# Kernel optimization log

Hardware: AMD Instinct MI355X
Metric: run time of the kernel (lower is better)

Reference implementation:

```python
import jax, jax.numpy as jnp
import numpy as np

N_NODES = 50000


def setup_inputs() -> dict:
    key = jax.random.key(0)
    k1, k2, k3, k4, k5, k6 = jax.random.split(key, 6)
    N, E, D, F = 50000, 800000, 512, 256
    feature_ori = jax.random.normal(k1, (N, D), dtype=jnp.float32)
    feature_aug = jax.random.normal(k2, (N, D), dtype=jnp.float32)
    edge_row = jax.random.randint(k3, (E,), 0, N, dtype=jnp.int32)
    edge_col = jax.random.randint(k4, (E,), 0, N, dtype=jnp.int32)
    edge_val = jax.random.uniform(k5, (E,), dtype=jnp.float32)
    # kaiming-uniform-ish init for weight, zeros for bias (as in reset_parameters)
    bound = float(np.sqrt(6.0 / D))
    weight = jax.random.uniform(k6, (D, F), dtype=jnp.float32, minval=-bound, maxval=bound)
    bias = jnp.zeros((F,), dtype=jnp.float32)
    return {
        "feature_ori": feature_ori,
        "feature_aug": feature_aug,
        "edge_row": edge_row,
        "edge_col": edge_col,
        "edge_val": edge_val,
        "weight": weight,
        "bias": bias,
    }


def _branch(feat, weight, bias, edge_row, edge_col, edge_val):
    # support = X @ W  -> [N, F]
    support = feat @ weight
    # sparse aggregation: out[i] = sum_{e: row[e]=i} val[e] * support[col[e]]
    msgs = edge_val[:, None] * support[edge_col]          # [E, F]
    out = jax.ops.segment_sum(msgs, edge_row, num_segments=N_NODES)
    return jax.nn.relu(out + bias)


def reference(feature_ori, feature_aug, edge_row, edge_col, edge_val, weight, bias):
    out_ori = _branch(feature_ori, weight, bias, edge_row, edge_col, edge_val)
    out_aug = _branch(feature_aug, weight, bias, edge_row, edge_col, edge_val)
    return (out_ori, out_aug)
```

## Files before the change

kernel.cpp:

```cpp
#include <hip/hip_runtime.h>
#include <hip/hip_bf16.h>

#define NNODES 50000
#define NEDGES 800000
#define DIN    512
#define FOUT   256

typedef __attribute__((ext_vector_type(8))) short short8;
typedef __attribute__((ext_vector_type(4))) float f32x4;
typedef __attribute__((ext_vector_type(4))) unsigned int u32x4;
typedef __attribute__((ext_vector_type(4))) unsigned short usv4;

static __device__ __forceinline__ unsigned short f2bf(float f) {
    unsigned int u = __float_as_uint(f);
    u += 0x7FFF + ((u >> 16) & 1);
    return (unsigned short)(u >> 16);
}
static __device__ __forceinline__ float bf2f(unsigned short h) {
    return __uint_as_float(((unsigned int)h) << 16);
}

__global__ void wt_convert(const float* __restrict__ W, unsigned short* __restrict__ Wt) {
    int o = blockIdx.x * 256 + threadIdx.x;
    int n = o >> 9, k = o & 511;
    Wt[o] = f2bf(W[k * FOUT + n]);
}

__global__ void hist_kernel(const int* __restrict__ row, int* __restrict__ cnt) {
    int e = blockIdx.x * 256 + threadIdx.x;
    if (e < NEDGES) atomicAdd(&cnt[row[e]], 1);
}

__global__ void scan_partial(const int* __restrict__ cnt, int* __restrict__ partial) {
    __shared__ int sm[256];
    int i = blockIdx.x * 256 + threadIdx.x;
    int v = (i < NNODES) ? cnt[i] : 0;
    sm[threadIdx.x] = v; __syncthreads();
    for (int s = 128; s > 0; s >>= 1) {
        if (threadIdx.x < s) sm[threadIdx.x] += sm[threadIdx.x + s];
        __syncthreads();
    }
    if (threadIdx.x == 0) partial[blockIdx.x] = sm[0];
}

__global__ void scan_exclusive_small(int* __restrict__ partial, int nb) {
    __shared__ int sm[256];
    int t = threadIdx.x;
    int v = (t < nb) ? partial[t] : 0;
    sm[t] = v; __syncthreads();
    for (int off = 1; off < 256; off <<= 1) {
        int add = (t >= off) ? sm[t - off] : 0;
        __syncthreads();
        sm[t] += add;
        __syncthreads();
    }
    if (t < nb) partial[t] = sm[t] - v;
}

__global__ void scan_write(const int* __restrict__ cnt, const int* __restrict__ partial,
                           int* __restrict__ row_start, int* __restrict__ cursor) {
    __shared__ int sm[256];
    int t = threadIdx.x;
    int i = blockIdx.x * 256 + t;
    int v = (i < NNODES) ? cnt[i] : 0;
    sm[t] = v; __syncthreads();
    for (int off = 1; off < 256; off <<= 1) {
        int add = (t >= off) ? sm[t - off] : 0;
        __syncthreads();
        sm[t] += add;
        __syncthreads();
    }
    if (i < NNODES) {
        int rs = partial[blockIdx.x] + sm[t] - v;
        row_start[i] = rs;
        cursor[i] = rs;
    }
    if (i == 0) row_start[NNODES] = NEDGES;
}

__global__ void scatter_kernel(const int* __restrict__ row, const int* __restrict__ col,
                               const float* __restrict__ val,
                               int* __restrict__ cursor, unsigned int* __restrict__ cv) {
    int e = blockIdx.x * 256 + threadIdx.x;
    if (e < NEDGES) {
        int r = row[e];
        int pos = atomicAdd(&cursor[r], 1);
        unsigned int vb = f2bf(val[e]);
        cv[pos] = (vb << 16) | (unsigned int)col[e];
    }
}

__global__ __launch_bounds__(512, 2)
void gemm_kernel(const float* __restrict__ Xo, const float* __restrict__ Xa,
                 const unsigned short* __restrict__ Wt,
                 unsigned short* __restrict__ S) {
    __shared__ __align__(16) unsigned short As[2][128][40];
    __shared__ __align__(16) unsigned short Bs[2][256][40];
    const int tid = threadIdx.x;
    const int branch = blockIdx.z;
    const float* __restrict__ X = branch ? Xa : Xo;
    const int boff = branch * 256;
    const int m_base = blockIdx.x * 128;
    const int lane = tid & 63, wave = tid >> 6;
    const int wm = (wave >> 2) * 64, wn = (wave & 3) * 64;
    const int quad = lane >> 4, r16 = lane & 15;

    f32x4 acc[4][4] = {};

    const int colf  = (tid & 7) * 4;
    const int rbase = tid >> 3;
    const int kseg  = (tid & 3) * 8;
    const int nrow  = tid >> 2;

    const int gm0 = m_base + rbase;
    const int gm1 = m_base + 64 + rbase;
    const bool va0 = gm0 < NNODES, va1 = gm1 < NNODES;
    const float* pA0 = &X[(long)gm0 * DIN + colf];
    const float* pA1 = &X[(long)gm1 * DIN + colf];
    const unsigned short* pB0 = &Wt[(long)nrow * DIN + kseg];
    const unsigned short* pB1 = &Wt[(long)(128 + nrow) * DIN + kseg];

    f32x4 fa0, fa1; u32x4 ub0, ub1;

#define GEMM_LOAD(K0)                                                          \
    do {                                                                       \
        fa0 = va0 ? __builtin_nontemporal_load((const f32x4*)(pA0 + (K0)))     \
                  : (f32x4)0.f;                                                \
        fa1 = va1 ? __builtin_nontemporal_load((const f32x4*)(pA1 + (K0)))     \
                  : (f32x4)0.f;                                                \
        ub0 = *(const u32x4*)(pB0 + (K0));                                     \
        ub1 = *(const u32x4*)(pB1 + (K0));                                     \
    } while (0)

#define GEMM_WRITE(B)                                                          \
    do {                                                                       \
        usv4 h0; h0.x = f2bf(fa0[0]); h0.y = f2bf(fa0[1]);                     \
        h0.z = f2bf(fa0[2]); h0.w = f2bf(fa0[3]);                              \
        *(usv4*)&As[B][rbase][colf] = h0;                                      \
        usv4 h1; h1.x = f2bf(fa1[0]); h1.y = f2bf(fa1[1]);                     \
        h1.z = f2bf(fa1[2]); h1.w = f2bf(fa1[3]);                              \
        *(usv4*)&As[B][64 + rbase][colf] = h1;                                 \
        *(u32x4*)&Bs[B][nrow][kseg] = ub0;                                     \
        *(u32x4*)&Bs[B][128 + nrow][kseg] = ub1;                               \
    } while (0)

#define GEMM_COMPUTE(B)                                                        \
    do {                                                                       \
        short8 a_frag[4], b_frag[4];                                           \
        _Pragma("unroll")                                                      \
        for (int mi = 0; mi < 4; mi++)                                         \
            a_frag[mi] = *(const short8*)&As[B][wm + mi * 16 + r16][quad * 8]; \
        _Pragma("unroll")                                                      \
        for (int ni = 0; ni < 4; ni++)                                         \
            b_frag[ni] = *(const short8*)&Bs[B][wn + ni * 16 + r16][quad * 8]; \
        _Pragma("unroll")                                                      \
        for (int mi = 0; mi < 4; mi++)                                         \
            _Pragma("unroll")                                                  \
            for (int ni = 0; ni < 4; ni++)                                     \
                acc[mi][ni] = __builtin_amdgcn_mfma_f32_16x16x32_bf16(         \
                    a_frag[mi], b_frag[ni], acc[mi][ni], 0, 0, 0);             \
    } while (0)

    GEMM_LOAD(0);
    GEMM_WRITE(0);
    __syncthreads();

    for (int k0 = 0; k0 < DIN; k0 += 64) {
        GEMM_LOAD(k0 + 32);
        GEMM_COMPUTE(0);
        GEMM_WRITE(1);
        __syncthreads();
        if (k0 + 64 < DIN) GEMM_LOAD(k0 + 64);
        GEMM_COMPUTE(1);
        if (k0 + 64 < DIN) GEMM_WRITE(0);
        __syncthreads();
    }

#undef GEMM_LOAD
#undef GEMM_WRITE
#undef GEMM_COMPUTE

    #pragma unroll
    for (int mi = 0; mi < 4; mi++) {
        #pragma unroll
        for (int rr = 0; rr < 4; rr++) {
            int m = m_base + wm + mi * 16 + quad * 4 + rr;
            if (m < NNODES) {
                #pragma unroll
                for (int ni = 0; ni < 4; ni++) {
                    int n = wn + ni * 16 + r16;
                    S[(long)m * 512 + boff + n] = f2bf(acc[mi][ni][rr]);
                }
            }
        }
    }
}

__global__ __launch_bounds__(256)
void aggregate_kernel(const int* __restrict__ row_start,
                      const unsigned int* __restrict__ cv,
                      const unsigned short* __restrict__ S,
                      const float* __restrict__ bias, float* __restrict__ out) {
    int node = blockIdx.x * 4 + (threadIdx.x >> 6);
    int lane = threadIdx.x & 63;
    if (node >= NNODES) return;
    int s = row_start[node], e = row_start[node + 1];
    float ao0 = 0.f, ao1 = 0.f, ao2 = 0.f, ao3 = 0.f;
    float aa0 = 0.f, aa1 = 0.f, aa2 = 0.f, aa3 = 0.f;
    const int lo = lane * 4;

    int idx = s;
    for (; idx + 4 <= e; idx += 4) {
        unsigned int w0 = __builtin_nontemporal_load(&cv[idx]);
        unsigned int w1 = __builtin_nontemporal_load(&cv[idx + 1]);
        unsigned int w2 = __builtin_nontemporal_load(&cv[idx + 2]);
        unsigned int w3 = __builtin_nontemporal_load(&cv[idx + 3]);
        const unsigned short* p0 = &S[(long)(w0 & 0xFFFFu) * 512 + lo];
        const unsigned short* p1 = &S[(long)(w1 & 0xFFFFu) * 512 + lo];
        const unsigned short* p2 = &S[(long)(w2 & 0xFFFFu) * 512 + lo];
        const unsigned short* p3 = &S[(long)(w3 & 0xFFFFu) * 512 + lo];
        usv4 po0 = *(const usv4*)p0;       usv4 pa0 = *(const usv4*)(p0 + 256);
        usv4 po1 = *(const usv4*)p1;       usv4 pa1 = *(const usv4*)(p1 + 256);
        usv4 po2 = *(const usv4*)p2;       usv4 pa2 = *(const usv4*)(p2 + 256);
        usv4 po3 = *(const usv4*)p3;       usv4 pa3 = *(const usv4*)(p3 + 256);
        float v0 = bf2f((unsigned short)(w0 >> 16));
        float v1 = bf2f((unsigned short)(w1 >> 16));
        float v2 = bf2f((unsigned short)(w2 >> 16));
        float v3 = bf2f((unsigned short)(w3 >> 16));
        ao0 += v0 * bf2f(po0.x); ao1 += v0 * bf2f(po0.y); ao2 += v0 * bf2f(po0.z); ao3 += v0 * bf2f(po0.w);
        aa0 += v0 * bf2f(pa0.x); aa1 += v0 * bf2f(pa0.y); aa2 += v0 * bf2f(pa0.z); aa3 += v0 * bf2f(pa0.w);
        ao0 += v1 * bf2f(po1.x); ao1 += v1 * bf2f(po1.y); ao2 += v1 * bf2f(po1.z); ao3 += v1 * bf2f(po1.w);
        aa0 += v1 * bf2f(pa1.x); aa1 += v1 * bf2f(pa1.y); aa2 += v1 * bf2f(pa1.z); aa3 += v1 * bf2f(pa1.w);
        ao0 += v2 * bf2f(po2.x); ao1 += v2 * bf2f(po2.y); ao2 += v2 * bf2f(po2.z); ao3 += v2 * bf2f(po2.w);
        aa0 += v2 * bf2f(pa2.x); aa1 += v2 * bf2f(pa2.y); aa2 += v2 * bf2f(pa2.z); aa3 += v2 * bf2f(pa2.w);
        ao0 += v3 * bf2f(po3.x); ao1 += v3 * bf2f(po3.y); ao2 += v3 * bf2f(po3.z); ao3 += v3 * bf2f(po3.w);
        aa0 += v3 * bf2f(pa3.x); aa1 += v3 * bf2f(pa3.y); aa2 += v3 * bf2f(pa3.z); aa3 += v3 * bf2f(pa3.w);
    }
    for (; idx < e; idx++) {
        unsigned int w = __builtin_nontemporal_load(&cv[idx]);
        const unsigned short* p = &S[(long)(w & 0xFFFFu) * 512 + lo];
        usv4 po = *(const usv4*)p;
        usv4 pa = *(const usv4*)(p + 256);
        float v = bf2f((unsigned short)(w >> 16));
        ao0 += v * bf2f(po.x); ao1 += v * bf2f(po.y); ao2 += v * bf2f(po.z); ao3 += v * bf2f(po.w);
        aa0 += v * bf2f(pa.x); aa1 += v * bf2f(pa.y); aa2 += v * bf2f(pa.z); aa3 += v * bf2f(pa.w);
    }

    f32x4 b = *(const f32x4*)&bias[lo];
    long o = (long)node * FOUT + lo;
    f32x4 ro, ra;
    ro[0] = fmaxf(ao0 + b[0], 0.f); ro[1] = fmaxf(ao1 + b[1], 0.f);
    ro[2] = fmaxf(ao2 + b[2], 0.f); ro[3] = fmaxf(ao3 + b[3], 0.f);
    ra[0] = fmaxf(aa0 + b[0], 0.f); ra[1] = fmaxf(aa1 + b[1], 0.f);
    ra[2] = fmaxf(aa2 + b[2], 0.f); ra[3] = fmaxf(aa3 + b[3], 0.f);
    __builtin_nontemporal_store(ro, (f32x4*)&out[o]);
    __builtin_nontemporal_store(ra, (f32x4*)&out[(long)NNODES * FOUT + o]);
}

extern "C" void kernel_launch(void* const* d_in, const int* in_sizes, int n_in,
                              void* d_out, int out_size, void* d_ws, size_t ws_size,
                              hipStream_t stream) {
    const float* Xo   = (const float*)d_in[0];
    const float* Xa   = (const float*)d_in[1];
    const int*   erow = (const int*)d_in[2];
    const int*   ecol = (const int*)d_in[3];
    const float* eval_= (const float*)d_in[4];
    const float* W    = (const float*)d_in[5];
    const float* bias = (const float*)d_in[6];
    float* out = (float*)d_out;

    char* ws = (char*)d_ws;
    unsigned short* S         = (unsigned short*)(ws);
    unsigned short* Wt        = (unsigned short*)(ws + 51200000);
    int*            cnt       = (int*)(ws + 51462144);
    int*            row_start = (int*)(ws + 51662144);
    int*            partial   = (int*)(ws + 51862208);
    unsigned int*   cv        = (unsigned int*)(ws + 51863232);

    (void)in_sizes; (void)n_in; (void)out_size; (void)ws_size;

    hipMemsetAsync(cnt, 0, 200000, stream);
    wt_convert<<<512, 256, 0, stream>>>(W, Wt);
    hist_kernel<<<3125, 256, 0, stream>>>(erow, cnt);
    scan_partial<<<196, 256, 0, stream>>>(cnt, partial);
    scan_exclusive_small<<<1, 256, 0, stream>>>(partial, 196);
    scan_write<<<196, 256, 0, stream>>>(cnt, partial, row_start, cnt);
    scatter_kernel<<<3125, 256, 0, stream>>>(erow, ecol, eval_, cnt, cv);

    dim3 gg(391, 1, 2);
    gemm_kernel<<<gg, 512, 0, stream>>>(Xo, Xa, Wt, S);

    aggregate_kernel<<<12500, 256, 0, stream>>>(row_start, cv, S, bias, out);
}
```

Measured before the change: 489.9 us.

## Software-pipeline aggregate gathers with 16-byte loads and merge prep kernels

Merges the weight conversion and the edge histogram into one launch to save a kernel launch. The aggregation kernel is restructured so each lane loads 8 bf16 values in one 16-byte load, with half the wave covering the ori branch and half the aug branch. It also double-buffers groups of four edge gathers so the next group's loads are issued before the current group's FMAs. This raises register use in exchange for more memory-level parallelism.

```diff
diff --git a/kernel.cpp b/kernel.cpp
--- a/kernel.cpp
+++ b/kernel.cpp
@@ -10,6 +10,7 @@
 typedef __attribute__((ext_vector_type(4))) float f32x4;
 typedef __attribute__((ext_vector_type(4))) unsigned int u32x4;
 typedef __attribute__((ext_vector_type(4))) unsigned short usv4;
+typedef __attribute__((ext_vector_type(8))) unsigned short usv8;
 
 static __device__ __forceinline__ unsigned short f2bf(float f) {
     unsigned int u = __float_as_uint(f);
@@ -20,15 +21,17 @@
     return __uint_as_float(((unsigned int)h) << 16);
 }
 
-__global__ void wt_convert(const float* __restrict__ W, unsigned short* __restrict__ Wt) {
-    int o = blockIdx.x * 256 + threadIdx.x;
-    int n = o >> 9, k = o & 511;
-    Wt[o] = f2bf(W[k * FOUT + n]);
-}
-
-__global__ void hist_kernel(const int* __restrict__ row, int* __restrict__ cnt) {
-    int e = blockIdx.x * 256 + threadIdx.x;
-    if (e < NEDGES) atomicAdd(&cnt[row[e]], 1);
+__global__ void prep_kernel(const float* __restrict__ W, unsigned short* __restrict__ Wt,
+                            const int* __restrict__ row, int* __restrict__ cnt) {
+    int b = blockIdx.x;
+    if (b < 512) {
+        int o = b * 256 + threadIdx.x;
+        int n = o >> 9, k = o & 511;
+        Wt[o] = f2bf(W[k * FOUT + n]);
+    } else {
+        int e = (b - 512) * 256 + threadIdx.x;
+        if (e < NEDGES) atomicAdd(&cnt[row[e]], 1);
+    }
 }
 
 __global__ void scan_partial(const int* __restrict__ cnt, int* __restrict__ partial) {
@@ -205,56 +208,80 @@
     int lane = threadIdx.x & 63;
     if (node >= NNODES) return;
     int s = row_start[node], e = row_start[node + 1];
-    float ao0 = 0.f, ao1 = 0.f, ao2 = 0.f, ao3 = 0.f;
-    float aa0 = 0.f, aa1 = 0.f, aa2 = 0.f, aa3 = 0.f;
-    const int lo = lane * 4;
+    const int f8 = (lane & 31) * 8;
+    const long soff = (long)(lane >> 5) * 256 + f8;
+    float a0 = 0.f, a1 = 0.f, a2 = 0.f, a3 = 0.f;
+    float a4 = 0.f, a5 = 0.f, a6 = 0.f, a7 = 0.f;
+
+#define LOADG(C0, C1, C2, C3, Q0, Q1, Q2, Q3, I)                               \
+    do {                                                                       \
+        C0 = __builtin_nontemporal_load(&cv[(I)]);                             \
+        C1 = __builtin_nontemporal_load(&cv[(I) + 1]);                         \
+        C2 = __builtin_nontemporal_load(&cv[(I) + 2]);                         \
+        C3 = __builtin_nontemporal_load(&cv[(I) + 3]);                         \
+        Q0 = *(const usv8*)&S[(long)(C0 & 0xFFFFu) * 512 + soff];              \
+        Q1 = *(const usv8*)&S[(long)(C1 & 0xFFFFu) * 512 + soff];              \
+        Q2 = *(const usv8*)&S[(long)(C2 & 0xFFFFu) * 512 + soff];              \
+        Q3 = *(const usv8*)&S[(long)(C3 & 0xFFFFu) * 512 + soff];              \
+    } while (0)
+
+#define EDGE_FMA(Cw, Q)                                                        \
+    do {                                                                       \
+        float v = bf2f((unsigned short)((Cw) >> 16));                          \
+        a0 = fmaf(v, bf2f((Q)[0]), a0); a1 = fmaf(v, bf2f((Q)[1]), a1);        \
+        a2 = fmaf(v, bf2f((Q)[2]), a2); a3 = fmaf(v, bf2f((Q)[3]), a3);        \
+        a4 = fmaf(v, bf2f((Q)[4]), a4); a5 = fmaf(v, bf2f((Q)[5]), a5);        \
+        a6 = fmaf(v, bf2f((Q)[6]), a6); a7 = fmaf(v, bf2f((Q)[7]), a7);        \
+    } while (0)
+
+#define FMAG(C0, C1, C2, C3, Q0, Q1, Q2, Q3)                                   \
+    do {                                                                       \
+        EDGE_FMA(C0, Q0); EDGE_FMA(C1, Q1);                                    \
+        EDGE_FMA(C2, Q2); EDGE_FMA(C3, Q3);                                    \
+    } while (0)
+
+    unsigned int c0, c1, c2, c3, d0, d1, d2, d3;
+    usv8 qa0, qa1, qa2, qa3, qb0, qb1, qb2, qb3;
 
     int idx = s;
-    for (; idx + 4 <= e; idx += 4) {
-        unsigned int w0 = __builtin_nontemporal_load(&cv[idx]);
-        unsigned int w1 = __builtin_nontemporal_load(&cv[idx + 1]);
-        unsigned int w2 = __builtin_nontemporal_load(&cv[idx + 2]);
-        unsigned int w3 = __builtin_nontemporal_load(&cv[idx + 3]);
-        const unsigned short* p0 = &S[(long)(w0 & 0xFFFFu) * 512 + lo];
-        const unsigned short* p1 = &S[(long)(w1 & 0xFFFFu) * 512 + lo];
-        const unsigned short* p2 = &S[(long)(w2 & 0xFFFFu) * 512 + lo];
-        const unsigned short* p3 = &S[(long)(w3 & 0xFFFFu) * 512 + lo];
-        usv4 po0 = *(const usv4*)p0;       usv4 pa0 = *(const usv4*)(p0 + 256);
-        usv4 po1 = *(const usv4*)p1;       usv4 pa1 = *(const usv4*)(p1 + 256);
-        usv4 po2 = *(const usv4*)p2;       usv4 pa2 = *(const usv4*)(p2 + 256);
-        usv4 po3 = *(const usv4*)p3;       usv4 pa3 = *(const usv4*)(p3 + 256);
-        float v0 = bf2f((unsigned short)(w0 >> 16));
-        float v1 = bf2f((unsigned short)(w1 >> 16));
-        float v2 = bf2f((unsigned short)(w2 >> 16));
-        float v3 = bf2f((unsigned short)(w3 >> 16));
-        ao0 += v0 * bf2f(po0.x); ao1 += v0 * bf2f(po0.y); ao2 += v0 * bf2f(po0.z); ao3 += v0 * bf2f(po0.w);
-        aa0 += v0 * bf2f(pa0.x); aa1 += v0 * bf2f(pa0.y); aa2 += v0 * bf2f(pa0.z); aa3 += v0 * bf2f(pa0.w);
-        ao0 += v1 * bf2f(po1.x); ao1 += v1 * bf2f(po1.y); ao2 += v1 * bf2f(po1.z); ao3 += v1 * bf2f(po1.w);
-        aa0 += v1 * bf2f(pa1.x); aa1 += v1 * bf2f(pa1.y); aa2 += v1 * bf2f(pa1.z); aa3 += v1 * bf2f(pa1.w);
-        ao0 += v2 * bf2f(po2.x); ao1 += v2 * bf2f(po2.y); ao2 += v2 * bf2f(po2.z); ao3 += v2 * bf2f(po2.w);
-        aa0 += v2 * bf2f(pa2.x); aa1 += v2 * bf2f(pa2.y); aa2 += v2 * bf2f(pa2.z); aa3 += v2 * bf2f(pa2.w);
-        ao0 += v3 * bf2f(po3.x); ao1 += v3 * bf2f(po3.y); ao2 += v3 * bf2f(po3.z); ao3 += v3 * bf2f(po3.w);
-        aa0 += v3 * bf2f(pa3.x); aa1 += v3 * bf2f(pa3.y); aa2 += v3 * bf2f(pa3.z); aa3 += v3 * bf2f(pa3.w);
+    int r = (e - s) >> 2;
+    if (r > 0) {
+        LOADG(c0, c1, c2, c3, qa0, qa1, qa2, qa3, idx); idx += 4; r--;
+        while (r >= 2) {
+            LOADG(d0, d1, d2, d3, qb0, qb1, qb2, qb3, idx); idx += 4;
+            FMAG(c0, c1, c2, c3, qa0, qa1, qa2, qa3);
+            LOADG(c0, c1, c2, c3, qa0, qa1, qa2, qa3, idx); idx += 4;
+            FMAG(d0, d1, d2, d3, qb0, qb1, qb2, qb3);
+            r -= 2;
+        }
+        if (r == 1) {
+            LOADG(d0, d1, d2, d3, qb0, qb1, qb2, qb3, idx); idx += 4;
+            FMAG(c0, c1, c2, c3, qa0, qa1, qa2, qa3);
+            FMAG(d0, d1, d2, d3, qb0, qb1, qb2, qb3);
+        } else {
+            FMAG(c0, c1, c2, c3, qa0, qa1, qa2, qa3);
+        }
     }
     for (; idx < e; idx++) {
         unsigned int w = __builtin_nontemporal_load(&cv[idx]);
-        const unsigned short* p = &S[(long)(w & 0xFFFFu) * 512 + lo];
-        usv4 po = *(const usv4*)p;
-        usv4 pa = *(const usv4*)(p + 256);
-        float v = bf2f((unsigned short)(w >> 16));
-        ao0 += v * bf2f(po.x); ao1 += v * bf2f(po.y); ao2 += v * bf2f(po.z); ao3 += v * bf2f(po.w);
-        aa0 += v * bf2f(pa.x); aa1 += v * bf2f(pa.y); aa2 += v * bf2f(pa.z); aa3 += v * bf2f(pa.w);
-    }
-
-    f32x4 b = *(const f32x4*)&bias[lo];
-    long o = (long)node * FOUT + lo;
-    f32x4 ro, ra;
-    ro[0] = fmaxf(ao0 + b[0], 0.f); ro[1] = fmaxf(ao1 + b[1], 0.f);
-    ro[2] = fmaxf(ao2 + b[2], 0.f); ro[3] = fmaxf(ao3 + b[3], 0.f);
-    ra[0] = fmaxf(aa0 + b[0], 0.f); ra[1] = fmaxf(aa1 + b[1], 0.f);
-    ra[2] = fmaxf(aa2 + b[2], 0.f); ra[3] = fmaxf(aa3 + b[3], 0.f);
-    __builtin_nontemporal_store(ro, (f32x4*)&out[o]);
-    __builtin_nontemporal_store(ra, (f32x4*)&out[(long)NNODES * FOUT + o]);
+        usv8 q = *(const usv8*)&S[(long)(w & 0xFFFFu) * 512 + soff];
+        EDGE_FMA(w, q);
+    }
+
+#undef LOADG
+#undef EDGE_FMA
+#undef FMAG
+
+    f32x4 b0 = *(const f32x4*)&bias[f8];
+    f32x4 b1 = *(const f32x4*)&bias[f8 + 4];
+    long o = (long)(lane >> 5) * NNODES * FOUT + (long)node * FOUT + f8;
+    f32x4 r0, r1;
+    r0[0] = fmaxf(a0 + b0[0], 0.f); r0[1] = fmaxf(a1 + b0[1], 0.f);
+    r0[2] = fmaxf(a2 + b0[2], 0.f); r0[3] = fmaxf(a3 + b0[3], 0.f);
+    r1[0] = fmaxf(a4 + b1[0], 0.f); r1[1] = fmaxf(a5 + b1[1], 0.f);
+    r1[2] = fmaxf(a6 + b1[2], 0.f); r1[3] = fmaxf(a7 + b1[3], 0.f);
+    __builtin_nontemporal_store(r0, (f32x4*)&out[o]);
+    __builtin_nontemporal_store(r1, (f32x4*)&out[o + 4]);
 }
 
 extern "C" void kernel_launch(void* const* d_in, const int* in_sizes, int n_in,
@@ -280,8 +307,7 @@
     (void)in_sizes; (void)n_in; (void)out_size; (void)ws_size;
 
     hipMemsetAsync(cnt, 0, 200000, stream);
-    wt_convert<<<512, 256, 0, stream>>>(W, Wt);
-    hist_kernel<<<3125, 256, 0, stream>>>(erow, cnt);
+    prep_kernel<<<3637, 256, 0, stream>>>(W, Wt, erow, cnt);
     scan_partial<<<196, 256, 0, stream>>>(cnt, partial);
     scan_exclusive_small<<<1, 256, 0, stream>>>(partial, 196);
     scan_write<<<196, 256, 0, stream>>>(cnt, partial, row_start, cnt);
```

New measurement: 487.0 us. Within noise of the previous version (-0.6%).
